# Kernel tuning notes

Hardware: AMD Instinct MI355X
Metric: run time of the kernel (lower is better)

Reference implementation:

```python
import jax, jax.numpy as jnp
import numpy as np

# ---- config (matches init_kwargs + VMamba/MambaIR SS2D defaults) ----
B, LEN, C, H, W = 2, 3, 64, 64, 64
N_STATE = 16           # d_state
D_INNER = 2 * C        # expand=2
DT_RANK = C // 16      # ceil(d_model/16)
K = 4                  # 4 scan directions
EPS = 1e-5


def _ln_last(x, g, b):
    m = x.mean(-1, keepdims=True)
    v = x.var(-1, keepdims=True)
    return (x - m) * jax.lax.rsqrt(v + EPS) * g + b


def _instance_ln(x):
    # kalman.utils.layer_norm: normalize each sample over (C,H,W), no affine
    m = x.mean(axis=(1, 2, 3), keepdims=True)
    v = x.var(axis=(1, 2, 3), keepdims=True)
    return (x - m) * jax.lax.rsqrt(v + EPS)


def _gn(x, g, b):
    # GroupNorm with num_groups=1 on NCHW
    m = x.mean(axis=(1, 2, 3), keepdims=True)
    v = x.var(axis=(1, 2, 3), keepdims=True)
    return (x - m) * jax.lax.rsqrt(v + EPS) * g[None, :, None, None] + b[None, :, None, None]


def _conv2d(x, w, b, groups=1):
    y = jax.lax.conv_general_dilated(x, w, (1, 1), 'SAME',
            dimension_numbers=('NCHW', 'OIHW', 'NCHW'), feature_group_count=groups)
    return y + b[None, :, None, None]


def _selective_scan(xs, dts, Bs, Cs, A, Ds, dt_bias):
    # xs, dts: (Bt,K,D,L); Bs, Cs: (Bt,K,N,L); A: (K,D,N); Ds, dt_bias: (K,D)
    delta = jax.nn.softplus(dts + dt_bias[None, :, :, None])
    u_t = jnp.moveaxis(xs, -1, 0)      # (L,Bt,K,D)
    d_t = jnp.moveaxis(delta, -1, 0)
    B_t = jnp.moveaxis(Bs, -1, 0)      # (L,Bt,K,N)
    C_t = jnp.moveaxis(Cs, -1, 0)
    h0 = jnp.zeros((xs.shape[0], K, xs.shape[2], A.shape[-1]), xs.dtype)

    def step(h, inp):
        u, d, Bv, Cv = inp
        dA = jnp.exp(d[..., None] * A)                                  # (Bt,K,D,N)
        h = dA * h + d[..., None] * Bv[:, :, None, :] * u[..., None]
        y = jnp.einsum('bkdn,bkn->bkd', h, Cv)
        return h, y

    _, ys = jax.lax.scan(step, h0, (u_t, d_t, B_t, C_t))
    ys = jnp.moveaxis(ys, 0, -1)                                        # (Bt,K,D,L)
    return ys + xs * Ds[None, :, :, None]


def _ss2d(x, in_proj_w, dwconv_w, dwconv_b, x_proj_w, dt_proj_w, dt_proj_b,
          A_logs, Ds, out_norm_g, out_norm_b, out_proj_w):
    Bt, Hh, Ww, Cc = x.shape
    L = Hh * Ww
    xz = x @ in_proj_w.T                               # (Bt,H,W,2*Di)
    xx, z = jnp.split(xz, 2, axis=-1)
    xx = jnp.transpose(xx, (0, 3, 1, 2))               # (Bt,Di,H,W)
    xx = jax.nn.silu(_conv2d(xx, dwconv_w, dwconv_b, groups=D_INNER))
    hw = xx.reshape(Bt, D_INNER, L)
    wh = jnp.transpose(xx, (0, 1, 3, 2)).reshape(Bt, D_INNER, L)
    xs = jnp.stack([hw, wh, hw[..., ::-1], wh[..., ::-1]], axis=1)      # (Bt,4,Di,L)
    x_dbl = jnp.einsum('bkdl,kcd->bkcl', xs, x_proj_w)
    dts = jnp.einsum('bkrl,kdr->bkdl', x_dbl[:, :, :DT_RANK], dt_proj_w)
    Bs = x_dbl[:, :, DT_RANK:DT_RANK + N_STATE]
    Cs = x_dbl[:, :, DT_RANK + N_STATE:]
    A = -jnp.exp(A_logs)                               # (K,Di,N)
    out_y = _selective_scan(xs, dts, Bs, Cs, A, Ds, dt_proj_b)
    inv = out_y[:, 2:4, :, ::-1]

    def wh2hw(y):
        return jnp.transpose(y.reshape(Bt, D_INNER, Ww, Hh), (0, 1, 3, 2)).reshape(Bt, D_INNER, L)

    y = out_y[:, 0] + inv[:, 0] + wh2hw(out_y[:, 1]) + wh2hw(inv[:, 1])
    y = jnp.transpose(y.reshape(Bt, D_INNER, Hh, Ww), (0, 2, 3, 1))
    y = _ln_last(y, out_norm_g, out_norm_b)
    y = y * jax.nn.silu(z)
    return y @ out_proj_w.T


def setup_inputs() -> dict:
    key = jax.random.key(0)
    ks = jax.random.split(key, 16)
    rn = lambda k, s, sc=0.05: jax.random.normal(k, s, jnp.float32) * sc
    inp = {}
    inp['image_sequence'] = jax.random.normal(ks[0], (B, LEN, C, H, W), jnp.float32)
    inp['difficult_zone'] = jax.random.normal(ks[1], (B, C, H, W), jnp.float32)
    inp['sigma'] = jax.random.uniform(ks[2], (B, C, H, W), jnp.float32)
    inp['gn1_g'] = jnp.ones((3 * C,)); inp['gn1_b'] = jnp.zeros((3 * C,))
    inp['conv1_w'] = rn(ks[3], (C, 3 * C, 3, 3)); inp['conv1_b'] = jnp.zeros((C,))
    inp['gn2_g'] = jnp.ones((C,)); inp['gn2_b'] = jnp.zeros((C,))
    inp['conv2_w'] = rn(ks[4], (C, C, 3, 3)); inp['conv2_b'] = jnp.zeros((C,))
    inp['skip_w'] = rn(ks[5], (C, 3 * C, 1, 1)); inp['skip_b'] = jnp.zeros((C,))
    inp['ln1_g'] = jnp.ones((C,)); inp['ln1_b'] = jnp.zeros((C,))
    inp['ln2_g'] = jnp.ones((C,)); inp['ln2_b'] = jnp.zeros((C,))
    inp['in_proj_w'] = rn(ks[6], (2 * D_INNER, C))
    inp['dwconv_w'] = rn(ks[7], (D_INNER, 1, 3, 3)); inp['dwconv_b'] = jnp.zeros((D_INNER,))
    inp['x_proj_w'] = rn(ks[8], (K, DT_RANK + 2 * N_STATE, D_INNER))
    inp['dt_proj_w'] = rn(ks[9], (K, D_INNER, DT_RANK), 0.2)
    inp['dt_proj_b'] = rn(ks[10], (K, D_INNER), 0.1)
    inp['A_logs'] = jnp.log(jnp.broadcast_to(jnp.arange(1, N_STATE + 1, dtype=jnp.float32), (K, D_INNER, N_STATE)))
    inp['Ds'] = jnp.ones((K, D_INNER))
    inp['out_norm_g'] = jnp.ones((D_INNER,)); inp['out_norm_b'] = jnp.zeros((D_INNER,))
    inp['out_proj_w'] = rn(ks[11], (C, D_INNER))
    inp['fc1_w'] = rn(ks[12], (C, C)); inp['fc1_b'] = jnp.zeros((C,))
    inp['fc2_w'] = rn(ks[13], (C, C)); inp['fc2_b'] = jnp.zeros((C,))
    return inp


def reference(image_sequence, difficult_zone, sigma,
              gn1_g, gn1_b, conv1_w, conv1_b, gn2_g, gn2_b, conv2_w, conv2_b, skip_w, skip_b,
              ln1_g, ln1_b, ln2_g, ln2_b,
              in_proj_w, dwconv_w, dwconv_b, x_proj_w, dt_proj_w, dt_proj_b,
              A_logs, Ds, out_norm_g, out_norm_b, out_proj_w,
              fc1_w, fc1_b, fc2_w, fc2_b):
    Bsz, Lf, Cc, Hh, Ww = image_sequence.shape
    # per-frame layer_norm; frames are independent so fold them into batch
    img = _instance_ln(image_sequence.reshape(Bsz * Lf, Cc, Hh, Ww)).reshape(Bsz, Lf, Cc, Hh, Ww)
    dz = jnp.broadcast_to(difficult_zone[:, None], (Bsz, Lf, Cc, Hh, Ww))
    sg = jnp.broadcast_to(sigma[:, None], (Bsz, Lf, Cc, Hh, Ww))
    x = jnp.concatenate([dz, img, sg], axis=2).reshape(Bsz * Lf, 3 * Cc, Hh, Ww)
    # ConvolutionalResBlock (GN -> SiLU -> conv, x2, + 1x1 skip)
    h = _conv2d(jax.nn.silu(_gn(x, gn1_g, gn1_b)), conv1_w, conv1_b)
    h = _conv2d(jax.nn.silu(_gn(h, gn2_g, gn2_b)), conv2_w, conv2_b)
    x = h + _conv2d(x, skip_w, skip_b)
    # VSSBlock (pre-norm): x + SS2D(LN(x)); x + Mlp(LN(x))
    x = jnp.transpose(x, (0, 2, 3, 1))                 # NHWC
    x = x + _ss2d(_ln_last(x, ln1_g, ln1_b), in_proj_w, dwconv_w, dwconv_b,
                  x_proj_w, dt_proj_w, dt_proj_b, A_logs, Ds,
                  out_norm_g, out_norm_b, out_proj_w)
    xm = _ln_last(x, ln2_g, ln2_b)
    x = x + (jax.nn.gelu(xm @ fc1_w.T + fc1_b) @ fc2_w.T + fc2_b)
    x = jnp.transpose(x, (0, 3, 1, 2)).reshape(Bsz, Lf, Cc, Hh, Ww)
    return x
```

## Files before the change

kernel.cpp:

```cpp
#include <hip/hip_runtime.h>
#include <hip/hip_bf16.h>

typedef unsigned short ushortT;
typedef short short8v __attribute__((ext_vector_type(8)));
typedef float float4v __attribute__((ext_vector_type(4)));

#define NBL 6
#define NC 64
#define NC3 192
#define NHW 4096
#define NDI 128
#define NNS 16
#define NDR 4
#define NK 4
#define NL 4096
#define NCH 128
#define SCLEN 32
#define NSTATE 49152

static const size_t F_XCAT  = 0;
static const size_t F_ACT1  = 4718592;
static const size_t F_H1    = 9437184;
static const size_t F_ACT2  = 11010048;
static const size_t F_H2    = 12582912;
static const size_t F_XRES  = 14155776;
static const size_t F_XXIN  = 15728640;
static const size_t F_Z     = 18874368;
static const size_t F_XXC   = 22020096;
static const size_t F_XDBL  = 25165824;
static const size_t F_YS    = 28704768;
static const size_t F_YCOMB = 41287680;
static const size_t F_X1    = 44433408;
static const size_t F_X2    = 46006272;
static const size_t F_STATS = 47579136;
static const size_t F_TOTAL = 47579184;

__device__ __forceinline__ float wred64(float v) {
#pragma unroll
  for (int m = 32; m; m >>= 1) v += __shfl_xor(v, m, 64);
  return v;
}

__device__ __forceinline__ float silu(float v) {
  return v / (1.f + __expf(-v));
}

__device__ __forceinline__ ushortT f2bf(float f) {
  unsigned int u = __builtin_bit_cast(unsigned int, f);
  unsigned int r = (u + 0x7FFFu + ((u >> 16) & 1u)) >> 16;
  return (ushortT)r;
}

__device__ __forceinline__ int map_pos(int k, int l) {
  if (k == 0) return l;
  if (k == 1) return ((l & 63) << 6) | (l >> 6);
  if (k == 2) return 4095 - l;
  int lp = 4095 - l;
  return ((lp & 63) << 6) | (lp >> 6);
}

__device__ __forceinline__ float softplus_fast(float a) {
  float t = exp2f(a * 1.44269504f);
  float r = 0.69314718f * __log2f(1.f + t);
  return (a > 20.f) ? a : r;
}

__device__ __forceinline__ void pow_tree(float E1, float4v& e0, float4v& e1,
                                         float4v& e2, float4v& e3) {
  float E2 = E1 * E1, E3 = E2 * E1, E4 = E2 * E2;
  float E5 = E4 * E1, E6 = E4 * E2, E7 = E4 * E3, E8 = E4 * E4;
  e0[0] = E1; e0[1] = E2; e0[2] = E3; e0[3] = E4;
  e1[0] = E5; e1[1] = E6; e1[2] = E7; e1[3] = E8;
  e2[0] = E8 * E1; e2[1] = E8 * E2; e2[2] = E8 * E3; e2[3] = E8 * E4;
  e3[0] = E8 * E5; e3[1] = E8 * E6; e3[2] = E8 * E7; e3[3] = E8 * E8;
}

__global__ __launch_bounds__(256) void wtrans_kernel(const float* __restrict__ src,
                                                     float* __restrict__ dst, int O, int C) {
  int id = blockIdx.x * 256 + threadIdx.x;
  if (id >= O * C) return;
  int c = id / O, o = id % O;
  dst[id] = src[o * C + c];
}

__global__ __launch_bounds__(256) void stats1_kernel(const float* __restrict__ in, int n,
                                                     double* __restrict__ part) {
  int bi = blockIdx.x;
  int s = bi >> 5, j = bi & 31;
  int slice = n >> 5;
  const float4* p = (const float4*)(in + (size_t)s * n + (size_t)j * slice);
  int n4 = slice >> 2;
  double dsum = 0.0, dsq = 0.0;
  for (int i = threadIdx.x; i < n4; i += 256) {
    float4 v = p[i];
    dsum += (double)((v.x + v.y) + (v.z + v.w));
    dsq += (double)v.x * v.x + (double)v.y * v.y + (double)v.z * v.z + (double)v.w * v.w;
  }
  __shared__ double s1[256], s2[256];
  s1[threadIdx.x] = dsum; s2[threadIdx.x] = dsq;
  __syncthreads();
  for (int off = 128; off; off >>= 1) {
    if (threadIdx.x < off) { s1[threadIdx.x] += s1[threadIdx.x + off]; s2[threadIdx.x] += s2[threadIdx.x + off]; }
    __syncthreads();
  }
  if (threadIdx.x == 0) { part[2 * bi] = s1[0]; part[2 * bi + 1] = s2[0]; }
}

__global__ __launch_bounds__(64) void stats2_kernel(const double* __restrict__ part, int n,
                                                    float* __restrict__ mean_out,
                                                    float* __restrict__ rstd_out) {
  int s = blockIdx.x;
  int lane = threadIdx.x;
  double sum = 0.0, sq = 0.0;
  if (lane < 32) { sum = part[2 * (s * 32 + lane)]; sq = part[2 * (s * 32 + lane) + 1]; }
#pragma unroll
  for (int m = 16; m; m >>= 1) { sum += __shfl_xor(sum, m, 64); sq += __shfl_xor(sq, m, 64); }
  if (lane == 0) {
    double mean = sum / n;
    double var = sq / n - mean * mean;
    mean_out[s] = (float)mean;
    rstd_out[s] = (float)(1.0 / sqrt(var + 1e-5));
  }
}

__global__ __launch_bounds__(256) void build_xcat_kernel(const float* __restrict__ img,
                                                         const float* __restrict__ dz,
                                                         const float* __restrict__ sg,
                                                         const float* __restrict__ stats,
                                                         float* __restrict__ xcat) {
  size_t gid = (size_t)blockIdx.x * 256 + threadIdx.x;
  int p = gid & 4095;
  size_t r = gid >> 12;
  int ch = (int)(r % NC3);
  int bl = (int)(r / NC3);
  int b = bl / 3;
  float v;
  if (ch < 64) {
    v = dz[((size_t)b * NC + ch) * NHW + p];
  } else if (ch < 128) {
    float m = stats[bl], rs = stats[8 + bl];
    v = (img[((size_t)bl * NC + (ch - 64)) * NHW + p] - m) * rs;
  } else {
    v = sg[((size_t)b * NC + (ch - 128)) * NHW + p];
  }
  xcat[gid] = v;
}

template <int CCH>
__global__ __launch_bounds__(256) void gnsilu_t_kernel(const float* __restrict__ in,
                                                       const float* __restrict__ g,
                                                       const float* __restrict__ b,
                                                       const float* __restrict__ stats,
                                                       ushortT* __restrict__ outb) {
  int bi = blockIdx.x;
  int bl = bi >> 6, h = bi & 63;
  __shared__ ushortT tile[CCH][66];
  float m = stats[bl], rs = stats[8 + bl];
  int t = threadIdx.x;
  for (int idx = t; idx < CCH * 64; idx += 256) {
    int ch = idx >> 6, w = idx & 63;
    float v = in[(((size_t)bl * CCH + ch) << 12) + (h << 6) + w];
    v = (v - m) * rs * g[ch] + b[ch];
    v = silu(v);
    tile[ch][w] = f2bf(v);
  }
  __syncthreads();
  constexpr int C8 = CCH / 8;
  for (int idx = t; idx < 64 * C8; idx += 256) {
    int w = idx / C8, c8 = idx % C8;
    short8v v;
#pragma unroll
    for (int j = 0; j < 8; ++j) v[j] = (short)tile[c8 * 8 + j][w];
    *(short8v*)&outb[(size_t)(bl * 4096 + h * 64 + w) * CCH + c8 * 8] = v;
  }
}

__global__ __launch_bounds__(256) void wprep_kernel(const float* __restrict__ w,
                                                    ushortT* __restrict__ out,
                                                    int CIN, int KT) {
  int id = blockIdx.x * 256 + threadIdx.x;
  int j = id & 7;
  int lane = (id >> 3) & 63;
  int nt = (id >> 9) & 3;
  int rest = id >> 11;
  int kt = rest % KT;
  int tap = rest / KT;
  int oc = nt * 16 + (lane & 15);
  int ic = kt * 32 + ((lane >> 4) << 3) + j;
  int r = tap / 3, s = tap % 3;
  out[id] = f2bf(w[(((size_t)oc * CIN + ic) * 3 + r) * 3 + s]);
}

template <int CIN>
__global__ __launch_bounds__(256) void conv_mfma_kernel(const ushortT* __restrict__ actb,
                                                        const ushortT* __restrict__ wb,
                                                        const float* __restrict__ bias,
                                                        float* __restrict__ out) {
  constexpr int KT = CIN / 32;
  constexpr int STRIDE = CIN + 8;
  constexpr int C8 = CIN / 8;
  int bi = blockIdx.x;
  int nh = bi & 1;
  int h = (bi >> 1) & 63;
  int bl = bi >> 7;
  int t = threadIdx.x;
  int wv = t >> 6, lane = t & 63;
  __shared__ ushortT lds[66 * STRIDE];
  float4v acc0 = {0.f, 0.f, 0.f, 0.f};
  float4v acc1 = {0.f, 0.f, 0.f, 0.f};
  int lrow = lane & 15;
  int lk = (lane >> 4) << 3;
  for (int dy = 0; dy < 3; ++dy) {
    int hh = h + dy - 1;
    bool valid = (hh >= 0) && (hh < 64);
    int hc = valid ? hh : 0;
    if (dy) __syncthreads();
    const ushortT* src = actb + (size_t)(bl * 4096 + hc * 64) * CIN;
    for (int idx = t; idx < 64 * C8; idx += 256) {
      int w = idx / C8, c8 = idx % C8;
      short8v v = {0, 0, 0, 0, 0, 0, 0, 0};
      if (valid) v = *(const short8v*)&src[(size_t)w * CIN + c8 * 8];
      *(short8v*)&lds[(w + 1) * STRIDE + c8 * 8] = v;
    }
    if (t < 2 * C8) {
      int which = t / C8, c8 = t % C8;
      short8v z = {0, 0, 0, 0, 0, 0, 0, 0};
      *(short8v*)&lds[(which ? 65 : 0) * STRIDE + c8 * 8] = z;
    }
    __syncthreads();
    for (int dx = 0; dx < 3; ++dx) {
      int tap = dy * 3 + dx;
      int wl = (wv << 4) + lrow + dx;
#pragma unroll
      for (int kt = 0; kt < KT; ++kt) {
        short8v a = *(const short8v*)&lds[wl * STRIDE + kt * 32 + lk];
        const ushortT* wp = wb + ((size_t)(((tap * KT + kt) * 4 + (nh << 1)) * 64 + lane) << 3);
        short8v b0 = *(const short8v*)&wp[0];
        short8v b1 = *(const short8v*)&wp[512];
        acc0 = __builtin_amdgcn_mfma_f32_16x16x32_bf16(a, b0, acc0, 0, 0, 0);
        acc1 = __builtin_amdgcn_mfma_f32_16x16x32_bf16(a, b1, acc1, 0, 0, 0);
      }
    }
  }
  int oc0 = (nh << 5) + lrow;
  int oc1 = oc0 + 16;
  int w0 = (wv << 4) + ((lane >> 4) << 2);
  float bv0 = bias[oc0], bv1 = bias[oc1];
  float4 o0 = make_float4(acc0[0] + bv0, acc0[1] + bv0, acc0[2] + bv0, acc0[3] + bv0);
  float4 o1 = make_float4(acc1[0] + bv1, acc1[1] + bv1, acc1[2] + bv1, acc1[3] + bv1);
  *(float4*)&out[(((size_t)bl * 64 + oc0) << 12) + (h << 6) + w0] = o0;
  *(float4*)&out[(((size_t)bl * 64 + oc1) << 12) + (h << 6) + w0] = o1;
}

__global__ __launch_bounds__(256) void skip_kernel(const float* __restrict__ xcat,
                                                   const float* __restrict__ h2,
                                                   const float* __restrict__ skwt,
                                                   const float* __restrict__ skb,
                                                   float* __restrict__ xres) {
  int bi = blockIdx.x;
  int bl = bi >> 6, h = bi & 63;
  int t = threadIdx.x;
  int oc = t & 63, w0 = (t >> 6) << 4;
  __shared__ float lds[64][64];
  float acc[16];
#pragma unroll
  for (int i = 0; i < 16; ++i) acc[i] = 0.f;
  for (int cc = 0; cc < 3; ++cc) {
    __syncthreads();
    for (int idx = t; idx < 4096; idx += 256) {
      int ch = idx >> 6, w = idx & 63;
      lds[ch][w] = xcat[(((size_t)bl * NC3 + cc * 64 + ch) << 12) + (h << 6) + w];
    }
    __syncthreads();
    for (int ch = 0; ch < 64; ++ch) {
      float wv = skwt[((cc << 6) + ch) * 64 + oc];
#pragma unroll
      for (int i = 0; i < 16; ++i) acc[i] += wv * lds[ch][w0 + i];
    }
  }
  float bv = skb[oc];
  int p0 = (h << 6) + w0;
#pragma unroll
  for (int i = 0; i < 16; ++i) {
    float hv = h2[(((size_t)bl * 64 + oc) << 12) + p0 + i];
    xres[((size_t)bl * NHW + p0 + i) * 64 + oc] = acc[i] + bv + hv;
  }
}

__global__ __launch_bounds__(256) void inproj_kernel(const float* __restrict__ xres,
                                                     const float* __restrict__ g,
                                                     const float* __restrict__ b,
                                                     const float* __restrict__ wt,
                                                     float* __restrict__ xxin,
                                                     float* __restrict__ z) {
  int wv = threadIdx.x >> 6, lane = threadIdx.x & 63;
  size_t pi0 = (size_t)blockIdx.x << 4;
  __shared__ float xb[64][16];
  float gv = g[lane], bv = b[lane];
#pragma unroll
  for (int j = 0; j < 4; ++j) {
    int p = (wv << 2) + j;
    float x = xres[(pi0 + p) * 64 + lane];
    float s = wred64(x);
    float s2 = wred64(x * x);
    float m = s * (1.f / 64), var = s2 * (1.f / 64) - m * m;
    float rstd = rsqrtf(var + 1e-5f);
    xb[lane][p] = (x - m) * rstd * gv + bv;
  }
  __syncthreads();
  int oc = (wv << 6) + lane;
  float4v a0 = {0.f, 0.f, 0.f, 0.f}, a1 = a0, a2 = a0, a3 = a0;
  for (int c = 0; c < 64; ++c) {
    float w = wt[(c << 8) + oc];
    const float4v* xr = (const float4v*)&xb[c][0];
    a0 += w * xr[0];
    a1 += w * xr[1];
    a2 += w * xr[2];
    a3 += w * xr[3];
  }
  float acc[16];
  *(float4v*)&acc[0] = a0;
  *(float4v*)&acc[4] = a1;
  *(float4v*)&acc[8] = a2;
  *(float4v*)&acc[12] = a3;
  float* dst = (oc < 128) ? xxin : z;
  int oco = (oc < 128) ? oc : (oc - 128);
#pragma unroll
  for (int p = 0; p < 16; ++p) dst[((pi0 + p) << 7) + oco] = acc[p];
}

__global__ __launch_bounds__(256) void dwconv_kernel(const float* __restrict__ xx,
                                                     const float* __restrict__ w,
                                                     const float* __restrict__ b,
                                                     float* __restrict__ out) {
  size_t gid = (size_t)blockIdx.x * 256 + threadIdx.x;
  int d = gid & 127;
  size_t pi = gid >> 7;
  int p = (int)(pi & 4095);
  int bl = (int)(pi >> 12);
  int h = p >> 6, wq = p & 63;
  float acc = b[d];
  const float* wr = w + d * 9;
#pragma unroll
  for (int dy = -1; dy <= 1; ++dy) {
    int hh = h + dy;
    if (hh < 0 || hh >= 64) continue;
#pragma unroll
    for (int dx = -1; dx <= 1; ++dx) {
      int ww = wq + dx;
      if (ww < 0 || ww >= 64) continue;
      acc += wr[(dy + 1) * 3 + (dx + 1)] * xx[(((size_t)bl << 12) + (hh << 6) + ww) * 128 + d];
    }
  }
  out[pi * 128 + d] = silu(acc);
}

__global__ __launch_bounds__(256) void xdbl_kernel(const float* __restrict__ xxc,
                                                   const float* __restrict__ xpw,
                                                   float* __restrict__ xdbl) {
  int bi = blockIdx.x;
  int lt = bi & 63;
  int k = (bi >> 6) & 3;
  int bl = bi >> 8;
  int lbase = lt << 6;
  __shared__ float lds[64][132];
  int t = threadIdx.x;
  for (int idx = t; idx < 64 * 128; idx += 256) {
    int i = idx >> 7, d = idx & 127;
    int pos = map_pos(k, lbase + i);
    lds[i][d] = xxc[((size_t)bl * NHW + pos) * 128 + d];
  }
  __syncthreads();
  for (int oi = t; oi < 36 * 64; oi += 256) {
    int c = oi >> 6, l = oi & 63;
    const float* wrow = xpw + (k * 36 + c) * 128;
    float acc = 0.f;
    for (int d4 = 0; d4 < 32; ++d4) {
      float4 w4 = *(const float4*)&wrow[d4 << 2];
      float4 x4 = *(const float4*)&lds[l][d4 << 2];
      acc += w4.x * x4.x + w4.y * x4.y + w4.z * x4.z + w4.w * x4.w;
    }
    xdbl[(((size_t)(bl * 4 + k)) * 36 + c) * (size_t)NL + lbase + l] = acc;
  }
}

__global__ __launch_bounds__(128) void scan_pass1_kernel(const float* __restrict__ xdbl,
                                                         const float* __restrict__ xxc,
                                                         const float* __restrict__ dtw,
                                                         const float* __restrict__ dtb,
                                                         const float* __restrict__ Alog,
                                                         float* __restrict__ chunkP,
                                                         float* __restrict__ chunkH) {
  int bi = blockIdx.x;
  int chunk = bi & (NCH - 1);
  int bk = bi >> 7;
  int k = bk & 3, bl = bk >> 2;
  int d = threadIdx.x;
  float4 wv = *(const float4*)(dtw + (size_t)(((k << 7) + d) << 2));
  float bias = dtb[(k << 7) + d];
  const float* ar = Alog + (size_t)(((k << 7) + d) << 4);
  float a1v = -__expf(ar[0]) * 1.44269504f;
  bool geom = true;
#pragma unroll
  for (int n = 1; n < 16; ++n) {
    float an = -__expf(ar[n]) * 1.44269504f;
    geom = geom && (fabsf(an - (float)(n + 1) * a1v) <= 1e-3f * fabsf((float)(n + 1) * a1v) + 1e-6f);
  }
  __shared__ float xd[SCLEN][20];
  int l0 = chunk << 5;
  for (int idx = threadIdx.x; idx < 20 * SCLEN; idx += 128) {
    int c = idx >> 5, li = idx & 31;
    xd[li][c] = xdbl[((size_t)bk * 36 + c) * (size_t)NL + l0 + li];
  }
  __syncthreads();
  const float* uB = xxc + ((size_t)bl << 19) + d;
  float4v h0 = {0.f, 0.f, 0.f, 0.f}, h1 = h0, h2 = h0, h3 = h0;
  float sdt = 0.f;
  float u_nxt = uB[(size_t)map_pos(k, l0) << 7];
  if (geom) {
    for (int li = 0; li < SCLEN; ++li) {
      float u = u_nxt;
      int nl = (li < SCLEN - 1) ? (li + 1) : (SCLEN - 1);
      u_nxt = uB[(size_t)map_pos(k, l0 + nl) << 7];
      const float4v* row = (const float4v*)&xd[li][0];
      float4v q0 = row[0];
      float accq = bias + wv.x * q0[0] + wv.y * q0[1] + wv.z * q0[2] + wv.w * q0[3];
      float dt = softplus_fast(accq);
      float dtu = dt * u;
      sdt += dt;
      float4v b0 = row[1], b1 = row[2], b2 = row[3], b3 = row[4];
      float4v e0, e1, e2, e3;
      pow_tree(exp2f(a1v * dt), e0, e1, e2, e3);
      h0 = e0 * h0 + dtu * b0;
      h1 = e1 * h1 + dtu * b1;
      h2 = e2 * h2 + dtu * b2;
      h3 = e3 * h3 + dtu * b3;
    }
  } else {
    float4v a0v, a1q, a2q, a3q;
#pragma unroll
    for (int j = 0; j < 4; ++j) {
      a0v[j] = -__expf(ar[j]) * 1.44269504f;
      a1q[j] = -__expf(ar[4 + j]) * 1.44269504f;
      a2q[j] = -__expf(ar[8 + j]) * 1.44269504f;
      a3q[j] = -__expf(ar[12 + j]) * 1.44269504f;
    }
    for (int li = 0; li < SCLEN; ++li) {
      float u = u_nxt;
      int nl = (li < SCLEN - 1) ? (li + 1) : (SCLEN - 1);
      u_nxt = uB[(size_t)map_pos(k, l0 + nl) << 7];
      const float4v* row = (const float4v*)&xd[li][0];
      float4v q0 = row[0];
      float accq = bias + wv.x * q0[0] + wv.y * q0[1] + wv.z * q0[2] + wv.w * q0[3];
      float dt = softplus_fast(accq);
      float dtu = dt * u;
      sdt += dt;
      float4v b0 = row[1], b1 = row[2], b2 = row[3], b3 = row[4];
      float4v e0, e1, e2, e3;
#pragma unroll
      for (int j = 0; j < 4; ++j) {
        e0[j] = exp2f(a0v[j] * dt);
        e1[j] = exp2f(a1q[j] * dt);
        e2[j] = exp2f(a2q[j] * dt);
        e3[j] = exp2f(a3q[j] * dt);
      }
      h0 = e0 * h0 + dtu * b0;
      h1 = e1 * h1 + dtu * b1;
      h2 = e2 * h2 + dtu * b2;
      h3 = e3 * h3 + dtu * b3;
    }
  }
  size_t base = (size_t)chunk * NSTATE + (((size_t)bk << 7) + (size_t)d) * 16;
  float4v p0, p1, p2, p3;
  if (geom) {
    pow_tree(exp2f(a1v * sdt), p0, p1, p2, p3);
  } else {
#pragma unroll
    for (int j = 0; j < 4; ++j) {
      p0[j] = exp2f(-__expf(ar[j]) * 1.44269504f * sdt);
      p1[j] = exp2f(-__expf(ar[4 + j]) * 1.44269504f * sdt);
      p2[j] = exp2f(-__expf(ar[8 + j]) * 1.44269504f * sdt);
      p3[j] = exp2f(-__expf(ar[12 + j]) * 1.44269504f * sdt);
    }
  }
  *(float4v*)&chunkP[base + 0] = p0;
  *(float4v*)&chunkP[base + 4] = p1;
  *(float4v*)&chunkP[base + 8] = p2;
  *(float4v*)&chunkP[base + 12] = p3;
  *(float4v*)&chunkH[base + 0] = h0;
  *(float4v*)&chunkH[base + 4] = h1;
  *(float4v*)&chunkH[base + 8] = h2;
  *(float4v*)&chunkH[base + 12] = h3;
}

__global__ __launch_bounds__(256) void scan_pass2_kernel(const float* __restrict__ chunkP,
                                                         const float* __restrict__ chunkH,
                                                         float* __restrict__ chunkHS) {
  size_t state = (size_t)blockIdx.x * 256 + threadIdx.x;
  float h = 0.f;
#pragma unroll 4
  for (int j = 0; j < NCH; ++j) {
    size_t idx = (size_t)j * NSTATE + state;
    chunkHS[idx] = h;
    h = chunkP[idx] * h + chunkH[idx];
  }
}

__global__ __launch_bounds__(128) void scan_pass3_kernel(const float* __restrict__ xdbl,
                                                         const float* __restrict__ xxc,
                                                         const float* __restrict__ dtw,
                                                         const float* __restrict__ dtb,
                                                         const float* __restrict__ Alog,
                                                         const float* __restrict__ chunkHS,
                                                         float* __restrict__ ys) {
  int bi = blockIdx.x;
  int chunk = bi & (NCH - 1);
  int bk = bi >> 7;
  int k = bk & 3, bl = bk >> 2;
  int d = threadIdx.x;
  float4 wv = *(const float4*)(dtw + (size_t)(((k << 7) + d) << 2));
  float bias = dtb[(k << 7) + d];
  const float* ar = Alog + (size_t)(((k << 7) + d) << 4);
  float a1v = -__expf(ar[0]) * 1.44269504f;
  bool geom = true;
#pragma unroll
  for (int n = 1; n < 16; ++n) {
    float an = -__expf(ar[n]) * 1.44269504f;
    geom = geom && (fabsf(an - (float)(n + 1) * a1v) <= 1e-3f * fabsf((float)(n + 1) * a1v) + 1e-6f);
  }
  __shared__ float xd[SCLEN][36];
  int l0 = chunk << 5;
  for (int idx = threadIdx.x; idx < 36 * SCLEN; idx += 128) {
    int c = idx >> 5, li = idx & 31;
    xd[li][c] = xdbl[((size_t)bk * 36 + c) * (size_t)NL + l0 + li];
  }
  __syncthreads();
  const float* uB = xxc + ((size_t)bl << 19) + d;
  float* yB = ys + ((size_t)bk << 19) + d;
  size_t base = (size_t)chunk * NSTATE + (((size_t)bk << 7) + (size_t)d) * 16;
  float4v h0 = *(const float4v*)&chunkHS[base + 0];
  float4v h1 = *(const float4v*)&chunkHS[base + 4];
  float4v h2 = *(const float4v*)&chunkHS[base + 8];
  float4v h3 = *(const float4v*)&chunkHS[base + 12];
  float u_nxt = uB[(size_t)map_pos(k, l0) << 7];
  if (geom) {
    for (int li = 0; li < SCLEN; ++li) {
      float u = u_nxt;
      int nl = (li < SCLEN - 1) ? (li + 1) : (SCLEN - 1);
      u_nxt = uB[(size_t)map_pos(k, l0 + nl) << 7];
      const float4v* row = (const float4v*)&xd[li][0];
      float4v q0 = row[0];
      float accq = bias + wv.x * q0[0] + wv.y * q0[1] + wv.z * q0[2] + wv.w * q0[3];
      float dt = softplus_fast(accq);
      float dtu = dt * u;
      float4v b0 = row[1], b1 = row[2], b2 = row[3], b3 = row[4];
      float4v c0 = row[5], c1 = row[6], c2 = row[7], c3 = row[8];
      float4v e0, e1, e2, e3;
      pow_tree(exp2f(a1v * dt), e0, e1, e2, e3);
      h0 = e0 * h0 + dtu * b0;
      h1 = e1 * h1 + dtu * b1;
      h2 = e2 * h2 + dtu * b2;
      h3 = e3 * h3 + dtu * b3;
      float4v sy = h0 * c0;
      sy += h1 * c1;
      sy += h2 * c2;
      sy += h3 * c3;
      yB[(size_t)(l0 + li) << 7] = (sy[0] + sy[1]) + (sy[2] + sy[3]);
    }
  } else {
    float4v a0v, a1q, a2q, a3q;
#pragma unroll
    for (int j = 0; j < 4; ++j) {
      a0v[j] = -__expf(ar[j]) * 1.44269504f;
      a1q[j] = -__expf(ar[4 + j]) * 1.44269504f;
      a2q[j] = -__expf(ar[8 + j]) * 1.44269504f;
      a3q[j] = -__expf(ar[12 + j]) * 1.44269504f;
    }
    for (int li = 0; li < SCLEN; ++li) {
      float u = u_nxt;
      int nl = (li < SCLEN - 1) ? (li + 1) : (SCLEN - 1);
      u_nxt = uB[(size_t)map_pos(k, l0 + nl) << 7];
      const float4v* row = (const float4v*)&xd[li][0];
      float4v q0 = row[0];
      float accq = bias + wv.x * q0[0] + wv.y * q0[1] + wv.z * q0[2] + wv.w * q0[3];
      float dt = softplus_fast(accq);
      float dtu = dt * u;
      float4v b0 = row[1], b1 = row[2], b2 = row[3], b3 = row[4];
      float4v c0 = row[5], c1 = row[6], c2 = row[7], c3 = row[8];
      float4v e0, e1, e2, e3;
#pragma unroll
      for (int j = 0; j < 4; ++j) {
        e0[j] = exp2f(a0v[j] * dt);
        e1[j] = exp2f(a1q[j] * dt);
        e2[j] = exp2f(a2q[j] * dt);
        e3[j] = exp2f(a3q[j] * dt);
      }
      h0 = e0 * h0 + dtu * b0;
      h1 = e1 * h1 + dtu * b1;
      h2 = e2 * h2 + dtu * b2;
      h3 = e3 * h3 + dtu * b3;
      float4v sy = h0 * c0;
      sy += h1 * c1;
      sy += h2 * c2;
      sy += h3 * c3;
      yB[(size_t)(l0 + li) << 7] = (sy[0] + sy[1]) + (sy[2] + sy[3]);
    }
  }
}

__global__ __launch_bounds__(256) void combine_kernel(const float* __restrict__ ys,
                                                      const float* __restrict__ xxc,
                                                      const float* __restrict__ Ds,
                                                      float* __restrict__ ycomb) {
  size_t gid = (size_t)blockIdx.x * 256 + threadIdx.x;
  int d = gid & 127;
  size_t pi = gid >> 7;
  int p = (int)(pi & 4095);
  int bl = (int)(pi >> 12);
  int h = p >> 6, w = p & 63;
  int l1 = (w << 6) | h;
  size_t base = ((size_t)bl * 4) << 12;
  float v = ys[((base + p) << 7) + d]
          + ys[((base + 4096 + l1) << 7) + d]
          + ys[((base + 2 * 4096 + (4095 - p)) << 7) + d]
          + ys[((base + 3 * 4096 + (4095 - l1)) << 7) + d];
  float ds = Ds[d] + Ds[128 + d] + Ds[256 + d] + Ds[384 + d];
  v += xxc[(pi << 7) + d] * ds;
  ycomb[(pi << 7) + d] = v;
}

__global__ __launch_bounds__(256) void outproj_kernel(const float* __restrict__ ycomb,
                                                      const float* __restrict__ z,
                                                      const float* __restrict__ ong,
                                                      const float* __restrict__ onb,
                                                      const float* __restrict__ opwt,
                                                      const float* __restrict__ xres,
                                                      float* __restrict__ x1) {
  int wv = threadIdx.x >> 6, lane = threadIdx.x & 63;
  size_t pi0 = (size_t)blockIdx.x << 4;
  __shared__ float gb[128][16];
  float og0 = ong[lane], ob0 = onb[lane];
  float og1 = ong[64 + lane], ob1 = onb[64 + lane];
#pragma unroll
  for (int j = 0; j < 4; ++j) {
    int p = (wv << 2) + j;
    size_t pp = pi0 + p;
    float y0 = ycomb[(pp << 7) + lane], y1 = ycomb[(pp << 7) + 64 + lane];
    float s = wred64(y0 + y1);
    float s2 = wred64(y0 * y0 + y1 * y1);
    float m = s * (1.f / 128), var = s2 * (1.f / 128) - m * m;
    float rstd = rsqrtf(var + 1e-5f);
    float z0 = z[(pp << 7) + lane], z1 = z[(pp << 7) + 64 + lane];
    gb[lane][p] = ((y0 - m) * rstd * og0 + ob0) * silu(z0);
    gb[64 + lane][p] = ((y1 - m) * rstd * og1 + ob1) * silu(z1);
  }
  __syncthreads();
  int p0 = wv << 2;
  float4v acc = {0.f, 0.f, 0.f, 0.f};
  for (int c = 0; c < 128; ++c) {
    float w = opwt[(c << 6) + lane];
    acc += w * (*(const float4v*)&gb[c][p0]);
  }
  float accs[4];
  *(float4v*)&accs[0] = acc;
#pragma unroll
  for (int j = 0; j < 4; ++j) {
    size_t pp = pi0 + p0 + j;
    x1[pp * 64 + lane] = xres[pp * 64 + lane] + accs[j];
  }
}

__global__ __launch_bounds__(256) void mlp_kernel(const float* __restrict__ x1,
                                                  const float* __restrict__ g2,
                                                  const float* __restrict__ b2,
                                                  const float* __restrict__ w1t,
                                                  const float* __restrict__ bb1,
                                                  const float* __restrict__ w2t,
                                                  const float* __restrict__ bb2,
                                                  float* __restrict__ x2) {
  int wv = threadIdx.x >> 6, lane = threadIdx.x & 63;
  size_t pi0 = (size_t)blockIdx.x << 4;
  __shared__ float xb[64][16], tb[64][16];
  float gv = g2[lane], bv = b2[lane];
  float xsave[4];
#pragma unroll
  for (int j = 0; j < 4; ++j) {
    int p = (wv << 2) + j;
    float xv = x1[(pi0 + p) * 64 + lane];
    xsave[j] = xv;
    float s = wred64(xv), s2 = wred64(xv * xv);
    float m = s * (1.f / 64), var = s2 * (1.f / 64) - m * m;
    float rstd = rsqrtf(var + 1e-5f);
    xb[lane][p] = (xv - m) * rstd * gv + bv;
  }
  __syncthreads();
  int p0 = wv << 2;
  float bb1v = bb1[lane];
  float4v acc = {bb1v, bb1v, bb1v, bb1v};
  for (int c = 0; c < 64; ++c) {
    float w = w1t[(c << 6) + lane];
    acc += w * (*(const float4v*)&xb[c][p0]);
  }
  float us[4];
  *(float4v*)&us[0] = acc;
#pragma unroll
  for (int j = 0; j < 4; ++j) {
    float u = us[j];
    float tt = tanhf(0.7978845608028654f * (u + 0.044715f * u * u * u));
    tb[lane][p0 + j] = 0.5f * u * (1.f + tt);
  }
  __syncthreads();
  float bb2v = bb2[lane];
  float4v acc2 = {bb2v, bb2v, bb2v, bb2v};
  for (int c = 0; c < 64; ++c) {
    float w = w2t[(c << 6) + lane];
    acc2 += w * (*(const float4v*)&tb[c][p0]);
  }
  float o2[4];
  *(float4v*)&o2[0] = acc2;
#pragma unroll
  for (int j = 0; j < 4; ++j)
    x2[(pi0 + p0 + j) * 64 + lane] = xsave[j] + o2[j];
}

__global__ __launch_bounds__(256) void transpose_out_kernel(const float* __restrict__ x2,
                                                            float* __restrict__ out) {
  int bi = blockIdx.x;
  int pt = bi & 127;
  int ct = (bi >> 7) & 1;
  int bl = bi >> 8;
  __shared__ float lds[32][33];
  int t = threadIdx.x;
  int j = t & 31, i0 = t >> 5;
  int p0 = pt << 5, c0 = ct << 5;
#pragma unroll
  for (int q = 0; q < 4; ++q) {
    int i = i0 + (q << 3);
    lds[i][j] = x2[((size_t)bl * NHW + p0 + i) * 64 + c0 + j];
  }
  __syncthreads();
#pragma unroll
  for (int q = 0; q < 4; ++q) {
    int i = i0 + (q << 3);
    out[((size_t)bl * 64 + c0 + i) * (size_t)NHW + p0 + j] = lds[j][i];
  }
}

extern "C" void kernel_launch(void* const* d_in, const int* in_sizes, int n_in,
                              void* d_out, int out_size, void* d_ws, size_t ws_size,
                              hipStream_t stream) {
  const float* img  = (const float*)d_in[0];
  const float* dz   = (const float*)d_in[1];
  const float* sg   = (const float*)d_in[2];
  const float* gn1g = (const float*)d_in[3];
  const float* gn1b = (const float*)d_in[4];
  const float* c1w  = (const float*)d_in[5];
  const float* c1b  = (const float*)d_in[6];
  const float* gn2g = (const float*)d_in[7];
  const float* gn2b = (const float*)d_in[8];
  const float* c2w  = (const float*)d_in[9];
  const float* c2b  = (const float*)d_in[10];
  const float* skw  = (const float*)d_in[11];
  const float* skb  = (const float*)d_in[12];
  const float* ln1g = (const float*)d_in[13];
  const float* ln1b = (const float*)d_in[14];
  const float* ln2g = (const float*)d_in[15];
  const float* ln2b = (const float*)d_in[16];
  const float* ipw  = (const float*)d_in[17];
  const float* dww  = (const float*)d_in[18];
  const float* dwb  = (const float*)d_in[19];
  const float* xpw  = (const float*)d_in[20];
  const float* dtw  = (const float*)d_in[21];
  const float* dtb  = (const float*)d_in[22];
  const float* Alog = (const float*)d_in[23];
  const float* Dsp  = (const float*)d_in[24];
  const float* ong  = (const float*)d_in[25];
  const float* onb  = (const float*)d_in[26];
  const float* opw  = (const float*)d_in[27];
  const float* f1w  = (const float*)d_in[28];
  const float* f1b  = (const float*)d_in[29];
  const float* f2w  = (const float*)d_in[30];
  const float* f2b  = (const float*)d_in[31];

  float* out = (float*)d_out;
  float* ws = (float*)d_ws;
  if (ws_size < F_TOTAL * sizeof(float)) return;

  float* xcat  = ws + F_XCAT;
  float* h1    = ws + F_H1;
  float* h2    = ws + F_H2;
  float* xres  = ws + F_XRES;
  float* xxin  = ws + F_XXIN;
  float* zbuf  = ws + F_Z;
  float* xxc   = ws + F_XXC;
  float* xdbl  = ws + F_XDBL;
  float* ysb   = ws + F_YS;
  float* ycomb = ws + F_YCOMB;
  float* x1    = ws + F_X1;
  float* x2    = ws + F_X2;
  float* stats = ws + F_STATS;
  ushortT* act1b = (ushortT*)(ws + F_ACT1);
  ushortT* act2b = (ushortT*)(ws + F_ACT2);
  double* part  = (double*)(ws + F_X2);
  ushortT* wb1  = (ushortT*)(ws + F_X2 + 1024);
  ushortT* wb2  = wb1 + 110592;
  float* chunkP  = ws + F_YS;
  float* chunkH  = ws + F_YS + 6291456;
  float* chunkHS = ws + F_XCAT;
  float* wt_sk = ws + F_ACT1;
  float* wt_ip = ws + F_XCAT;
  float* wt_op = ws + F_XXIN;
  float* wt_f1 = ws + F_XXIN + 8192;
  float* wt_f2 = ws + F_XXIN + 12288;

  wprep_kernel<<<432, 256, 0, stream>>>(c1w, wb1, NC3, 6);
  wprep_kernel<<<144, 256, 0, stream>>>(c2w, wb2, NC, 2);
  stats1_kernel<<<NBL * 32, 256, 0, stream>>>(img, NC * NHW, part);
  stats2_kernel<<<NBL, 64, 0, stream>>>(part, NC * NHW, stats + 0, stats + 8);
  build_xcat_kernel<<<18432, 256, 0, stream>>>(img, dz, sg, stats, xcat);
  stats1_kernel<<<NBL * 32, 256, 0, stream>>>(xcat, NC3 * NHW, part);
  stats2_kernel<<<NBL, 64, 0, stream>>>(part, NC3 * NHW, stats + 16, stats + 24);
  gnsilu_t_kernel<NC3><<<NBL * 64, 256, 0, stream>>>(xcat, gn1g, gn1b, stats + 16, act1b);
  conv_mfma_kernel<NC3><<<NBL * 64 * 2, 256, 0, stream>>>(act1b, wb1, c1b, h1);
  wtrans_kernel<<<48, 256, 0, stream>>>(skw, wt_sk, 64, 192);
  stats1_kernel<<<NBL * 32, 256, 0, stream>>>(h1, NC * NHW, part);
  stats2_kernel<<<NBL, 64, 0, stream>>>(part, NC * NHW, stats + 32, stats + 40);
  gnsilu_t_kernel<NC><<<NBL * 64, 256, 0, stream>>>(h1, gn2g, gn2b, stats + 32, act2b);
  conv_mfma_kernel<NC><<<NBL * 64 * 2, 256, 0, stream>>>(act2b, wb2, c2b, h2);
  skip_kernel<<<NBL * 64, 256, 0, stream>>>(xcat, h2, wt_sk, skb, xres);
  wtrans_kernel<<<64, 256, 0, stream>>>(ipw, wt_ip, 256, 64);
  inproj_kernel<<<1536, 256, 0, stream>>>(xres, ln1g, ln1b, wt_ip, xxin, zbuf);
  dwconv_kernel<<<12288, 256, 0, stream>>>(xxin, dww, dwb, xxc);
  wtrans_kernel<<<32, 256, 0, stream>>>(opw, wt_op, 64, 128);
  wtrans_kernel<<<16, 256, 0, stream>>>(f1w, wt_f1, 64, 64);
  wtrans_kernel<<<16, 256, 0, stream>>>(f2w, wt_f2, 64, 64);
  xdbl_kernel<<<NBL * NK * 64, 256, 0, stream>>>(xxc, xpw, xdbl);
  scan_pass1_kernel<<<24 * NCH, 128, 0, stream>>>(xdbl, xxc, dtw, dtb, Alog, chunkP, chunkH);
  scan_pass2_kernel<<<192, 256, 0, stream>>>(chunkP, chunkH, chunkHS);
  scan_pass3_kernel<<<24 * NCH, 128, 0, stream>>>(xdbl, xxc, dtw, dtb, Alog, chunkHS, ysb);
  combine_kernel<<<12288, 256, 0, stream>>>(ysb, xxc, Dsp, ycomb);
  outproj_kernel<<<1536, 256, 0, stream>>>(ycomb, zbuf, ong, onb, wt_op, xres, x1);
  mlp_kernel<<<1536, 256, 0, stream>>>(x1, ln2g, ln2b, wt_f1, f1b, wt_f2, f2b, x2);
  transpose_out_kernel<<<NBL * 256, 256, 0, stream>>>(x2, out);
}
```

Before: 404.0 us.

## Share xdbl input tiles between reversed scan directions and register-block outputs

The x_proj kernel now loads each 64-position tile once and computes both a forward direction and its reversed counterpart (k and k+2) from the same LDS tile, halving the grid and the global input loads. Each wave computes 18 output channels per position in registers, with weights read via uniform loads, instead of one dot product per thread. LDS uses an XOR swizzle in place of padding to avoid bank conflicts. The reversed directions are written to mirrored output positions, which relies on direction k+2 being the exact reverse of direction k.

```diff
diff --git a/kernel.cpp b/kernel.cpp
--- a/kernel.cpp
+++ b/kernel.cpp
@@ -360,28 +360,44 @@
                                                    float* __restrict__ xdbl) {
   int bi = blockIdx.x;
   int lt = bi & 63;
-  int k = (bi >> 6) & 3;
-  int bl = bi >> 8;
+  int korder = (bi >> 6) & 1;
+  int bl = bi >> 7;
   int lbase = lt << 6;
-  __shared__ float lds[64][132];
+  __shared__ float xs[64 * 128];
   int t = threadIdx.x;
-  for (int idx = t; idx < 64 * 128; idx += 256) {
-    int i = idx >> 7, d = idx & 127;
-    int pos = map_pos(k, lbase + i);
-    lds[i][d] = xxc[((size_t)bl * NHW + pos) * 128 + d];
-  }
-  __syncthreads();
-  for (int oi = t; oi < 36 * 64; oi += 256) {
-    int c = oi >> 6, l = oi & 63;
-    const float* wrow = xpw + (k * 36 + c) * 128;
-    float acc = 0.f;
-    for (int d4 = 0; d4 < 32; ++d4) {
-      float4 w4 = *(const float4*)&wrow[d4 << 2];
-      float4 x4 = *(const float4*)&lds[l][d4 << 2];
-      acc += w4.x * x4.x + w4.y * x4.y + w4.z * x4.z + w4.w * x4.w;
-    }
-    xdbl[(((size_t)(bl * 4 + k)) * 36 + c) * (size_t)NL + lbase + l] = acc;
-  }
+#pragma unroll
+  for (int it = 0; it < 8; ++it) {
+    int idx = it * 256 + t;
+    int i = idx >> 5, d4 = idx & 31;
+    int l = lbase + i;
+    int pos = korder ? (((l & 63) << 6) | (l >> 6)) : l;
+    float4 v = *(const float4*)&xxc[((size_t)bl * NHW + pos) * 128 + (d4 << 2)];
+    int slot = d4 ^ (i & 7);
+    *(float4*)&xs[i * 128 + (slot << 2)] = v;
+  }
+  __syncthreads();
+  int wv = __builtin_amdgcn_readfirstlane(t >> 6);
+  int lane = t & 63;
+  int k_w = korder + ((wv >= 2) ? 2 : 0);
+  int c0 = (wv & 1) * 18;
+  float acc[18];
+#pragma unroll
+  for (int j = 0; j < 18; ++j) acc[j] = 0.f;
+  const float* wbase = xpw + (size_t)(k_w * 36 + c0) * 128;
+  for (int d4 = 0; d4 < 32; ++d4) {
+    int slot = d4 ^ (lane & 7);
+    float4 x4 = *(const float4*)&xs[lane * 128 + (slot << 2)];
+#pragma unroll
+    for (int j = 0; j < 18; ++j) {
+      float4 w4 = *(const float4*)&wbase[j * 128 + (d4 << 2)];
+      acc[j] += w4.x * x4.x + w4.y * x4.y + w4.z * x4.z + w4.w * x4.w;
+    }
+  }
+  int lout = (k_w < 2) ? (lbase + lane) : (4095 - lbase - lane);
+  size_t obase = ((size_t)(bl * 4 + k_w) * 36 + c0) * (size_t)NL + lout;
+#pragma unroll
+  for (int j = 0; j < 18; ++j)
+    xdbl[obase + (size_t)j * NL] = acc[j];
 }
 
 __global__ __launch_bounds__(128) void scan_pass1_kernel(const float* __restrict__ xdbl,
@@ -834,7 +850,7 @@
   wtrans_kernel<<<32, 256, 0, stream>>>(opw, wt_op, 64, 128);
   wtrans_kernel<<<16, 256, 0, stream>>>(f1w, wt_f1, 64, 64);
   wtrans_kernel<<<16, 256, 0, stream>>>(f2w, wt_f2, 64, 64);
-  xdbl_kernel<<<NBL * NK * 64, 256, 0, stream>>>(xxc, xpw, xdbl);
+  xdbl_kernel<<<NBL * 2 * 64, 256, 0, stream>>>(xxc, xpw, xdbl);
   scan_pass1_kernel<<<24 * NCH, 128, 0, stream>>>(xdbl, xxc, dtw, dtb, Alog, chunkP, chunkH);
   scan_pass2_kernel<<<192, 256, 0, stream>>>(chunkP, chunkH, chunkHS);
   scan_pass3_kernel<<<24 * NCH, 128, 0, stream>>>(xdbl, xxc, dtw, dtb, Alog, chunkHS, ysb);
```

New measurement: 355.1 us. -12.1%, faster.
